# Kernel tuning notes

Measured on AMD Instinct MI355X. Metric: run time of the kernel, lower is better.

Reference implementation:

```python
import jax, jax.numpy as jnp
import numpy as np

N_HEAD, D_MODEL, D_K, D_V, POS_DIM = 8, 512, 64, 64, 2
TEMPERATURE = 8.0
LN_EPS = 1e-6


def setup_inputs() -> dict:
    key = jax.random.key(0)
    ks = jax.random.split(key, 16)
    B, S = 4, 1024
    s = 0.02
    return {
        "q": jax.random.normal(ks[0], (B, S, D_MODEL), jnp.float32),
        "k": jax.random.normal(ks[1], (B, S, D_MODEL), jnp.float32),
        "v": jax.random.normal(ks[2], (B, S, D_MODEL), jnp.float32),
        "pos_mat": jax.random.normal(ks[3], (S, S, POS_DIM), jnp.float32),
        "w_qs": jax.random.normal(ks[4], (N_HEAD * D_K, D_MODEL), jnp.float32) * s,
        "w_ks": jax.random.normal(ks[5], (N_HEAD * D_K, D_MODEL), jnp.float32) * s,
        "w_vs": jax.random.normal(ks[6], (N_HEAD * D_V, D_MODEL), jnp.float32) * s,
        "w_fc": jax.random.normal(ks[7], (D_MODEL, N_HEAD * D_V), jnp.float32) * s,
        "rp_w1": jax.random.normal(ks[8], (D_K, POS_DIM), jnp.float32) * s,
        "rp_b1": jnp.zeros((D_K,), jnp.float32),
        "rp_w2": jax.random.normal(ks[9], (D_K, D_K), jnp.float32) * s,
        "rp_b2": jnp.zeros((D_K,), jnp.float32),
        "ln_g": jnp.ones((D_MODEL,), jnp.float32),
        "ln_b": jnp.zeros((D_MODEL,), jnp.float32),
    }


def reference(q, k, v, pos_mat, w_qs, w_ks, w_vs, w_fc, rp_w1, rp_b1, rp_w2, rp_b2, ln_g, ln_b):
    B, S, _ = q.shape
    residual = q
    # projections -> (b, h, s, d)
    Q = (q @ w_qs.T).reshape(B, S, N_HEAD, D_K).transpose(0, 2, 1, 3)
    K = (k @ w_ks.T).reshape(B, S, N_HEAD, D_K).transpose(0, 2, 1, 3)
    V = (v @ w_vs.T).reshape(B, S, N_HEAD, D_V).transpose(0, 2, 1, 3)
    # relative position embedding: (s, s, d_k)
    a_k = jnp.tanh  # placeholder name avoided; compute MLP (no nonlinearity in original)
    a_k = (pos_mat @ rp_w1.T + rp_b1) @ rp_w2.T + rp_b2
    # sum over d_k of elementwise q*k*a_k, without materializing (b,h,q,k,d)
    attn = jnp.einsum("bhqd,bhkd,qkd->bhqk", Q, K, a_k) / TEMPERATURE
    attn = jax.nn.softmax(attn, axis=-1)  # dropout disabled (eval)
    out = jnp.einsum("bhqk,bhkd->bhqd", attn, V)  # (b,h,s,d_v)
    out = out.transpose(0, 2, 1, 3).reshape(B, S, N_HEAD * D_V)
    out = out @ w_fc.T + residual
    # layer norm
    mu = out.mean(-1, keepdims=True)
    var = out.var(-1, keepdims=True)
    out = (out - mu) / jnp.sqrt(var + LN_EPS) * ln_g + ln_b
    return (out, attn)
```

## Files before the change

### kernel.cpp

```cpp
#include <hip/hip_runtime.h>
#include <math.h>

#define NB   4
#define SEQ  1024
#define DMOD 512
#define NHD  8
#define DK   64

typedef unsigned short ushort_t;
typedef __attribute__((ext_vector_type(8))) short bf16x8;
typedef __attribute__((ext_vector_type(4))) float f32x4;

#define XQ_OFF   1024
#define XK_OFF   (XQ_OFF + 4194304)
#define XV_OFF   (XK_OFF + 4194304)
#define WQ_OFF   (XV_OFF + 4194304)
#define WK_OFF   (WQ_OFF + 524288)
#define WV_OFF   (WK_OFF + 524288)
#define WF_OFF   (WV_OFF + 524288)
#define QBF_OFF  (WF_OFF + 524288)
#define KBF_OFF  (QBF_OFF + 4194304)
#define VT_OFF   (KBF_OFF + 12582912)
#define O2_OFF   XQ_OFF
#define OBF_OFF  XV_OFF
#define POSBF_OFF XQ_OFF

__device__ inline ushort_t f2bf(float x) {
    unsigned u = __builtin_bit_cast(unsigned, x);
    unsigned r = (u + 0x7FFFu + ((u >> 16) & 1u)) >> 16;
    return (ushort_t)r;
}
__device__ inline unsigned pk2(float a, float b) {
    return (unsigned)f2bf(a) | ((unsigned)f2bf(b) << 16);
}

__global__ __launch_bounds__(64)
void prep_kernel(const float* __restrict__ rp_w1, const float* __restrict__ rp_b1,
                 const float* __restrict__ rp_w2, const float* __restrict__ rp_b2,
                 float* __restrict__ ws)
{
    int d = threadIdx.x;
    float w0 = 0.f, w1 = 0.f, cc = 0.f;
    for (int j = 0; j < 64; j++) {
        float r2 = rp_w2[d * 64 + j];
        w0 += r2 * rp_w1[j * 2 + 0];
        w1 += r2 * rp_w1[j * 2 + 1];
        cc += r2 * rp_b1[j];
    }
    ws[d] = cc + rp_b2[d];
    ws[64 + 2 * d + 0] = w0;
    ws[64 + 2 * d + 1] = w1;
}

__global__ __launch_bounds__(256)
void cvt3_kernel(const float* __restrict__ s0, const float* __restrict__ s1,
                 const float* __restrict__ s2, ushort_t* __restrict__ d0,
                 ushort_t* __restrict__ d1, ushort_t* __restrict__ d2)
{
    int t = blockIdx.x * 256 + threadIdx.x;
    const float* s = (blockIdx.y == 0) ? s0 : (blockIdx.y == 1) ? s1 : s2;
    ushort_t* d = (blockIdx.y == 0) ? d0 : (blockIdx.y == 1) ? d1 : d2;
    float4 v = *(const float4*)&s[t * 4];
    uint2 o = {pk2(v.x, v.y), pk2(v.z, v.w)};
    *(uint2*)&d[t * 4] = o;
}

__global__ __launch_bounds__(256)
void cvt4_kernel(const float* __restrict__ s0, const float* __restrict__ s1,
                 const float* __restrict__ s2, const float* __restrict__ s3,
                 ushort_t* __restrict__ d0, ushort_t* __restrict__ d1,
                 ushort_t* __restrict__ d2, ushort_t* __restrict__ d3)
{
    int t = blockIdx.x * 256 + threadIdx.x;
    const float* s = (blockIdx.y == 0) ? s0 : (blockIdx.y == 1) ? s1
                   : (blockIdx.y == 2) ? s2 : s3;
    ushort_t* d = (blockIdx.y == 0) ? d0 : (blockIdx.y == 1) ? d1
                : (blockIdx.y == 2) ? d2 : d3;
    float4 v = *(const float4*)&s[t * 4];
    uint2 o = {pk2(v.x, v.y), pk2(v.z, v.w)};
    *(uint2*)&d[t * 4] = o;
}

__global__ __launch_bounds__(256)
void poscvt_kernel(const float* __restrict__ pos, unsigned* __restrict__ posbf)
{
    int t = blockIdx.x * 256 + threadIdx.x;
    float4 a = *(const float4*)&pos[t * 8];
    float4 b = *(const float4*)&pos[t * 8 + 4];
    uint4 o = {pk2(a.x, a.y), pk2(a.z, a.w), pk2(b.x, b.y), pk2(b.z, b.w)};
    *(uint4*)&posbf[t * 4] = o;
}

#define GP 72
template<int MODE>
__global__ __launch_bounds__(256)
void mfma_gemm(const ushort_t* __restrict__ X, const ushort_t* __restrict__ Wt,
               ushort_t* __restrict__ obf, float* __restrict__ ofp,
               const float* __restrict__ wc, const float* __restrict__ resid)
{
    __shared__ ushort_t Xs[64 * GP];
    __shared__ ushort_t Ws[64 * GP];
    const int n0 = blockIdx.y * 64;
    const int o0 = blockIdx.x * 64;
    const int tid = threadIdx.x;
    const int wave = tid >> 6, lane = tid & 63;
    const int m16 = lane & 15, g = lane >> 4;

    f32x4 acc[4] = {};
    for (int m0 = 0; m0 < 512; m0 += 64) {
        #pragma unroll
        for (int it = 0; it < 2; it++) {
            int idx = tid + it * 256;
            int row = idx >> 3, c8 = (idx & 7) * 8;
            *(uint4*)&Xs[row * GP + c8] = *(const uint4*)&X[(n0 + row) * 512 + m0 + c8];
            *(uint4*)&Ws[row * GP + c8] = *(const uint4*)&Wt[(o0 + row) * 512 + m0 + c8];
        }
        __syncthreads();
        #pragma unroll
        for (int kc = 0; kc < 2; kc++) {
            bf16x8 a = *(const bf16x8*)&Xs[(wave * 16 + m16) * GP + kc * 32 + g * 8];
            #pragma unroll
            for (int to = 0; to < 4; to++) {
                bf16x8 b = *(const bf16x8*)&Ws[(to * 16 + m16) * GP + kc * 32 + g * 8];
                acc[to] = __builtin_amdgcn_mfma_f32_16x16x32_bf16(a, b, acc[to], 0, 0, 0);
            }
        }
        __syncthreads();
    }
    #pragma unroll
    for (int to = 0; to < 4; to++) {
        int o = o0 + to * 16 + m16;
        #pragma unroll
        for (int r = 0; r < 4; r++) {
            int n = n0 + wave * 16 + g * 4 + r;
            float a = acc[to][r];
            int b = n >> 10, s = n & 1023, h = o >> 6, d = o & 63;
            if (MODE == 0) {
                obf[(((b * NHD + h) << 10) + s) * 64 + d] = f2bf(a);
            } else if (MODE == 1) {
                int base = ((((b * NHD + h) << 10) + s) * 192) + d;
                obf[base]       = f2bf(a * wc[d]);
                obf[base + 64]  = f2bf(a * wc[64 + 2 * d + 0]);
                obf[base + 128] = f2bf(a * wc[64 + 2 * d + 1]);
            } else if (MODE == 2) {
                obf[((b * NHD + h) * 64 + d) * 1024 + s] = f2bf(a);
            } else {
                ofp[n * 512 + o] = a + resid[n * 512 + o];
            }
        }
    }
}

#define QPITCH 72
#define KPLANE (64 * QPITCH + 8)
#define POSP 68
__global__ __launch_bounds__(256)
void fused_attn(const ushort_t* __restrict__ Qbf, const ushort_t* __restrict__ Kbf,
                const unsigned* __restrict__ posu, const ushort_t* __restrict__ Vt,
                float* __restrict__ attn, ushort_t* __restrict__ Obf)
{
    __shared__ ushort_t Ks[3 * KPLANE];
    __shared__ ushort_t Vs[64 * QPITCH];
    __shared__ ushort_t Ps[64 * QPITCH];
    __shared__ unsigned PosS[64 * POSP];
    const int bh = blockIdx.x;
    const int q0 = blockIdx.y * 64;
    const int tid = threadIdx.x;
    const int wave = tid >> 6, lane = tid & 63;
    const int m16 = lane & 15, g = lane >> 4;

    const ushort_t* qrow = &Qbf[((bh << 10) + q0 + wave * 16 + m16) * 64];
    bf16x8 qf0 = *(const bf16x8*)&qrow[g * 8];
    bf16x8 qf1 = *(const bf16x8*)&qrow[32 + g * 8];

    float l[4] = {0.f, 0.f, 0.f, 0.f};

    for (int k0 = 0; k0 < 1024; k0 += 64) {
        #pragma unroll
        for (int it = 0; it < 6; it++) {
            int idx = tid + it * 256;
            int row = idx / 24, c = idx % 24;
            int j = c >> 3, d8 = (c & 7) * 8;
            *(uint4*)&Ks[j * KPLANE + row * QPITCH + d8] =
                *(const uint4*)&Kbf[((bh << 10) + k0 + row) * 192 + c * 8];
        }
        #pragma unroll
        for (int it = 0; it < 4; it++) {
            int idx = tid + it * 256;
            int row = idx >> 4, c4 = (idx & 15) * 4;
            *(uint4*)&PosS[row * POSP + c4] =
                *(const uint4*)&posu[(q0 + row) * 1024 + k0 + c4];
        }
        __syncthreads();

        f32x4 sc[4][3] = {};
        #pragma unroll
        for (int kc = 0; kc < 2; kc++) {
            bf16x8 af = kc ? qf1 : qf0;
            #pragma unroll
            for (int tk = 0; tk < 4; tk++)
                #pragma unroll
                for (int j = 0; j < 3; j++) {
                    bf16x8 bfv = *(const bf16x8*)&Ks[j * KPLANE + (tk * 16 + m16) * QPITCH + kc * 32 + g * 8];
                    sc[tk][j] = __builtin_amdgcn_mfma_f32_16x16x32_bf16(af, bfv, sc[tk][j], 0, 0, 0);
                }
        }

        #pragma unroll
        for (int r = 0; r < 4; r++) {
            #pragma unroll
            for (int tk = 0; tk < 4; tk++) {
                unsigned pu = PosS[(wave * 16 + g * 4 + r) * POSP + tk * 16 + m16];
                float p0 = __builtin_bit_cast(float, pu << 16);
                float p1 = __builtin_bit_cast(float, pu & 0xFFFF0000u);
                float s = (sc[tk][0][r] + p0 * sc[tk][1][r] + p1 * sc[tk][2][r]) * 0.125f;
                l[r] += __expf(s);
            }
        }
        __syncthreads();
    }
    float inv_l[4];
    #pragma unroll
    for (int r = 0; r < 4; r++) {
        float s = l[r];
        #pragma unroll
        for (int msk = 1; msk < 16; msk <<= 1) s += __shfl_xor(s, msk, 64);
        inv_l[r] = 1.0f / s;
    }

    f32x4 ao[4] = {};
    for (int k0 = 0; k0 < 1024; k0 += 64) {
        #pragma unroll
        for (int it = 0; it < 6; it++) {
            int idx = tid + it * 256;
            int row = idx / 24, c = idx % 24;
            int j = c >> 3, d8 = (c & 7) * 8;
            *(uint4*)&Ks[j * KPLANE + row * QPITCH + d8] =
                *(const uint4*)&Kbf[((bh << 10) + k0 + row) * 192 + c * 8];
        }
        #pragma unroll
        for (int it = 0; it < 2; it++) {
            int idx = tid + it * 256;
            int row = idx >> 3, c8 = (idx & 7) * 8;
            *(uint4*)&Vs[row * QPITCH + c8] = *(const uint4*)&Vt[(bh * 64 + row) * 1024 + k0 + c8];
        }
        #pragma unroll
        for (int it = 0; it < 4; it++) {
            int idx = tid + it * 256;
            int row = idx >> 4, c4 = (idx & 15) * 4;
            *(uint4*)&PosS[row * POSP + c4] =
                *(const uint4*)&posu[(q0 + row) * 1024 + k0 + c4];
        }
        __syncthreads();

        f32x4 sc[4][3] = {};
        #pragma unroll
        for (int kc = 0; kc < 2; kc++) {
            bf16x8 af = kc ? qf1 : qf0;
            #pragma unroll
            for (int tk = 0; tk < 4; tk++)
                #pragma unroll
                for (int j = 0; j < 3; j++) {
                    bf16x8 bfv = *(const bf16x8*)&Ks[j * KPLANE + (tk * 16 + m16) * QPITCH + kc * 32 + g * 8];
                    sc[tk][j] = __builtin_amdgcn_mfma_f32_16x16x32_bf16(af, bfv, sc[tk][j], 0, 0, 0);
                }
        }

        #pragma unroll
        for (int r = 0; r < 4; r++) {
            int q = q0 + wave * 16 + g * 4 + r;
            #pragma unroll
            for (int tk = 0; tk < 4; tk++) {
                unsigned pu = PosS[(wave * 16 + g * 4 + r) * POSP + tk * 16 + m16];
                float p0 = __builtin_bit_cast(float, pu << 16);
                float p1 = __builtin_bit_cast(float, pu & 0xFFFF0000u);
                float s = (sc[tk][0][r] + p0 * sc[tk][1][r] + p1 * sc[tk][2][r]) * 0.125f;
                float p = __expf(s) * inv_l[r];
                attn[((bh << 10) + q) * 1024 + k0 + tk * 16 + m16] = p;
                Ps[(wave * 16 + g * 4 + r) * QPITCH + tk * 16 + m16] = f2bf(p);
            }
        }
        __syncthreads();

        #pragma unroll
        for (int kc = 0; kc < 2; kc++) {
            bf16x8 a = *(const bf16x8*)&Ps[(wave * 16 + m16) * QPITCH + kc * 32 + g * 8];
            #pragma unroll
            for (int td = 0; td < 4; td++) {
                bf16x8 b = *(const bf16x8*)&Vs[(td * 16 + m16) * QPITCH + kc * 32 + g * 8];
                ao[td] = __builtin_amdgcn_mfma_f32_16x16x32_bf16(a, b, ao[td], 0, 0, 0);
            }
        }
        __syncthreads();
    }

    const int b = bh >> 3, h = bh & 7;
    #pragma unroll
    for (int td = 0; td < 4; td++) {
        int d = td * 16 + m16;
        #pragma unroll
        for (int r = 0; r < 4; r++) {
            int q = q0 + wave * 16 + g * 4 + r;
            Obf[((b << 10) + q) * 512 + h * 64 + d] = f2bf(ao[td][r]);
        }
    }
}

__global__ __launch_bounds__(256)
void ln_kernel(const float* __restrict__ X, const float* __restrict__ g,
               const float* __restrict__ bta, float* __restrict__ out)
{
    const int row = blockIdx.x;
    const int tid = threadIdx.x;
    float2 x = *(const float2*)&X[row * 512 + tid * 2];
    float s  = x.x + x.y;
    float s2 = x.x * x.x + x.y * x.y;
    for (int off = 32; off; off >>= 1) {
        s  += __shfl_down(s, off, 64);
        s2 += __shfl_down(s2, off, 64);
    }
    __shared__ float rs[4], rs2[4];
    __shared__ float mu_s, rstd_s;
    int wave = tid >> 6, lane = tid & 63;
    if (lane == 0) { rs[wave] = s; rs2[wave] = s2; }
    __syncthreads();
    if (tid == 0) {
        float S1 = rs[0] + rs[1] + rs[2] + rs[3];
        float S2 = rs2[0] + rs2[1] + rs2[2] + rs2[3];
        float mu = S1 * (1.0f / 512.0f);
        float var = S2 * (1.0f / 512.0f) - mu * mu;
        mu_s = mu;
        rstd_s = rsqrtf(var + 1e-6f);
    }
    __syncthreads();
    float mu = mu_s, rstd = rstd_s;
    float2 gv = *(const float2*)&g[tid * 2];
    float2 bv = *(const float2*)&bta[tid * 2];
    float2 o;
    o.x = (x.x - mu) * rstd * gv.x + bv.x;
    o.y = (x.y - mu) * rstd * gv.y + bv.y;
    *(float2*)&out[row * 512 + tid * 2] = o;
}

extern "C" void kernel_launch(void* const* d_in, const int* in_sizes, int n_in,
                              void* d_out, int out_size, void* d_ws, size_t ws_size,
                              hipStream_t stream)
{
    const float* q       = (const float*)d_in[0];
    const float* k       = (const float*)d_in[1];
    const float* v       = (const float*)d_in[2];
    const float* pos_mat = (const float*)d_in[3];
    const float* w_qs    = (const float*)d_in[4];
    const float* w_ks    = (const float*)d_in[5];
    const float* w_vs    = (const float*)d_in[6];
    const float* w_fc    = (const float*)d_in[7];
    const float* rp_w1   = (const float*)d_in[8];
    const float* rp_b1   = (const float*)d_in[9];
    const float* rp_w2   = (const float*)d_in[10];
    const float* rp_b2   = (const float*)d_in[11];
    const float* ln_g    = (const float*)d_in[12];
    const float* ln_b    = (const float*)d_in[13];

    char* wsb = (char*)d_ws;
    float*    wc  = (float*)d_ws;
    ushort_t* XQ  = (ushort_t*)(wsb + XQ_OFF);
    ushort_t* XK  = (ushort_t*)(wsb + XK_OFF);
    ushort_t* XV  = (ushort_t*)(wsb + XV_OFF);
    ushort_t* WQ  = (ushort_t*)(wsb + WQ_OFF);
    ushort_t* WK  = (ushort_t*)(wsb + WK_OFF);
    ushort_t* WV  = (ushort_t*)(wsb + WV_OFF);
    ushort_t* WF  = (ushort_t*)(wsb + WF_OFF);
    ushort_t* Qbf = (ushort_t*)(wsb + QBF_OFF);
    ushort_t* Kbf = (ushort_t*)(wsb + KBF_OFF);
    ushort_t* Vt  = (ushort_t*)(wsb + VT_OFF);
    float*    O2  = (float*)(wsb + O2_OFF);
    ushort_t* Obf = (ushort_t*)(wsb + OBF_OFF);
    unsigned* Pbf = (unsigned*)(wsb + POSBF_OFF);

    float* out  = (float*)d_out;
    float* attn = out + 2097152;

    prep_kernel<<<dim3(1), dim3(64), 0, stream>>>(rp_w1, rp_b1, rp_w2, rp_b2, wc);

    cvt3_kernel<<<dim3(2048, 3), 256, 0, stream>>>(q, k, v, XQ, XK, XV);
    cvt4_kernel<<<dim3(256, 4), 256, 0, stream>>>(w_qs, w_ks, w_vs, w_fc, WQ, WK, WV, WF);

    dim3 gp(8, 64);
    mfma_gemm<0><<<gp, 256, 0, stream>>>(XQ, WQ, Qbf, nullptr, nullptr, nullptr);
    poscvt_kernel<<<dim3(1024), 256, 0, stream>>>(pos_mat, Pbf);
    mfma_gemm<1><<<gp, 256, 0, stream>>>(XK, WK, Kbf, nullptr, wc, nullptr);
    mfma_gemm<2><<<gp, 256, 0, stream>>>(XV, WV, Vt, nullptr, nullptr, nullptr);

    fused_attn<<<dim3(32, 16), 256, 0, stream>>>(Qbf, Kbf, Pbf, Vt, attn, Obf);

    mfma_gemm<3><<<gp, 256, 0, stream>>>(Obf, WF, nullptr, O2, nullptr, q);
    ln_kernel<<<dim3(4096), 256, 0, stream>>>(O2, ln_g, ln_b, out);
}
```

Before: 303.1 us.

## Prefetch next K/pos/V tiles into registers while computing the current tile

```diff
diff --git a/kernel.cpp b/kernel.cpp
--- a/kernel.cpp
+++ b/kernel.cpp
@@ -169,29 +169,69 @@
     const int wave = tid >> 6, lane = tid & 63;
     const int m16 = lane & 15, g = lane >> 4;
 
+    const int k_row = (tid % 192) / 24 + (tid / 192) * 8;
+    (void)k_row;
+
     const ushort_t* qrow = &Qbf[((bh << 10) + q0 + wave * 16 + m16) * 64];
     bf16x8 qf0 = *(const bf16x8*)&qrow[g * 8];
     bf16x8 qf1 = *(const bf16x8*)&qrow[32 + g * 8];
 
+    uint4 kreg[6], preg[4], vreg[2];
+
+#define LOAD_K(k0_) \
+    _Pragma("unroll") \
+    for (int it = 0; it < 6; it++) { \
+        int idx = tid + it * 256; \
+        int row = idx / 24, c = idx % 24; \
+        kreg[it] = *(const uint4*)&Kbf[((bh << 10) + (k0_) + row) * 192 + c * 8]; \
+    }
+#define LOAD_P(k0_) \
+    _Pragma("unroll") \
+    for (int it = 0; it < 4; it++) { \
+        int idx = tid + it * 256; \
+        int row = idx >> 4, c4 = (idx & 15) * 4; \
+        preg[it] = *(const uint4*)&posu[(q0 + row) * 1024 + (k0_) + c4]; \
+    }
+#define LOAD_V(k0_) \
+    _Pragma("unroll") \
+    for (int it = 0; it < 2; it++) { \
+        int idx = tid + it * 256; \
+        int row = idx >> 3, c8 = (idx & 7) * 8; \
+        vreg[it] = *(const uint4*)&Vt[(bh * 64 + row) * 1024 + (k0_) + c8]; \
+    }
+#define STORE_K() \
+    _Pragma("unroll") \
+    for (int it = 0; it < 6; it++) { \
+        int idx = tid + it * 256; \
+        int row = idx / 24, c = idx % 24; \
+        int j = c >> 3, d8 = (c & 7) * 8; \
+        *(uint4*)&Ks[j * KPLANE + row * QPITCH + d8] = kreg[it]; \
+    }
+#define STORE_P() \
+    _Pragma("unroll") \
+    for (int it = 0; it < 4; it++) { \
+        int idx = tid + it * 256; \
+        int row = idx >> 4, c4 = (idx & 15) * 4; \
+        *(uint4*)&PosS[row * POSP + c4] = preg[it]; \
+    }
+#define STORE_V() \
+    _Pragma("unroll") \
+    for (int it = 0; it < 2; it++) { \
+        int idx = tid + it * 256; \
+        int row = idx >> 3, c8 = (idx & 7) * 8; \
+        *(uint4*)&Vs[row * QPITCH + c8] = vreg[it]; \
+    }
+
     float l[4] = {0.f, 0.f, 0.f, 0.f};
 
+    LOAD_K(0); LOAD_P(0);
+    STORE_K(); STORE_P();
+    __syncthreads();
     for (int k0 = 0; k0 < 1024; k0 += 64) {
-        #pragma unroll
-        for (int it = 0; it < 6; it++) {
-            int idx = tid + it * 256;
-            int row = idx / 24, c = idx % 24;
-            int j = c >> 3, d8 = (c & 7) * 8;
-            *(uint4*)&Ks[j * KPLANE + row * QPITCH + d8] =
-                *(const uint4*)&Kbf[((bh << 10) + k0 + row) * 192 + c * 8];
-        }
-        #pragma unroll
-        for (int it = 0; it < 4; it++) {
-            int idx = tid + it * 256;
-            int row = idx >> 4, c4 = (idx & 15) * 4;
-            *(uint4*)&PosS[row * POSP + c4] =
-                *(const uint4*)&posu[(q0 + row) * 1024 + k0 + c4];
-        }
-        __syncthreads();
+        const int kn = k0 + 64;
+        if (kn < 1024) {
+            LOAD_K(kn); LOAD_P(kn);
+        }
 
         f32x4 sc[4][3] = {};
         #pragma unroll
@@ -218,6 +258,10 @@
             }
         }
         __syncthreads();
+        if (kn < 1024) {
+            STORE_K(); STORE_P();
+        }
+        __syncthreads();
     }
     float inv_l[4];
     #pragma unroll
@@ -227,31 +271,17 @@
         for (int msk = 1; msk < 16; msk <<= 1) s += __shfl_xor(s, msk, 64);
         inv_l[r] = 1.0f / s;
     }
+    __syncthreads();
 
     f32x4 ao[4] = {};
+    LOAD_K(0); LOAD_P(0); LOAD_V(0);
+    STORE_K(); STORE_P(); STORE_V();
+    __syncthreads();
     for (int k0 = 0; k0 < 1024; k0 += 64) {
-        #pragma unroll
-        for (int it = 0; it < 6; it++) {
-            int idx = tid + it * 256;
-            int row = idx / 24, c = idx % 24;
-            int j = c >> 3, d8 = (c & 7) * 8;
-            *(uint4*)&Ks[j * KPLANE + row * QPITCH + d8] =
-                *(const uint4*)&Kbf[((bh << 10) + k0 + row) * 192 + c * 8];
-        }
-        #pragma unroll
-        for (int it = 0; it < 2; it++) {
-            int idx = tid + it * 256;
-            int row = idx >> 3, c8 = (idx & 7) * 8;
-            *(uint4*)&Vs[row * QPITCH + c8] = *(const uint4*)&Vt[(bh * 64 + row) * 1024 + k0 + c8];
-        }
-        #pragma unroll
-        for (int it = 0; it < 4; it++) {
-            int idx = tid + it * 256;
-            int row = idx >> 4, c4 = (idx & 15) * 4;
-            *(uint4*)&PosS[row * POSP + c4] =
-                *(const uint4*)&posu[(q0 + row) * 1024 + k0 + c4];
-        }
-        __syncthreads();
+        const int kn = k0 + 64;
+        if (kn < 1024) {
+            LOAD_K(kn); LOAD_P(kn); LOAD_V(kn);
+        }
 
         f32x4 sc[4][3] = {};
         #pragma unroll
@@ -292,6 +322,10 @@
             }
         }
         __syncthreads();
+        if (kn < 1024) {
+            STORE_K(); STORE_P(); STORE_V();
+        }
+        __syncthreads();
     }
 
     const int b = bh >> 3, h = bh & 7;
@@ -304,6 +338,12 @@
             Obf[((b << 10) + q) * 512 + h * 64 + d] = f2bf(ao[td][r]);
         }
     }
+#undef LOAD_K
+#undef LOAD_P
+#undef LOAD_V
+#undef STORE_K
+#undef STORE_P
+#undef STORE_V
 }
 
 __global__ __launch_bounds__(256)
```

Result: slower. 413.6 us (+36.4%).

## Fuse fp32-to-bf16 input conversion into a single batched QKV projection GEMM

Applied to the files above, without the earlier changes.

```diff
diff --git a/kernel.cpp b/kernel.cpp
--- a/kernel.cpp
+++ b/kernel.cpp
@@ -21,9 +21,9 @@
 #define QBF_OFF  (WF_OFF + 524288)
 #define KBF_OFF  (QBF_OFF + 4194304)
 #define VT_OFF   (KBF_OFF + 12582912)
+#define POSBF_OFF XQ_OFF
 #define O2_OFF   XQ_OFF
 #define OBF_OFF  XV_OFF
-#define POSBF_OFF XQ_OFF
 
 __device__ inline ushort_t f2bf(float x) {
     unsigned u = __builtin_bit_cast(unsigned, x);
@@ -50,19 +50,6 @@
     ws[d] = cc + rp_b2[d];
     ws[64 + 2 * d + 0] = w0;
     ws[64 + 2 * d + 1] = w1;
-}
-
-__global__ __launch_bounds__(256)
-void cvt3_kernel(const float* __restrict__ s0, const float* __restrict__ s1,
-                 const float* __restrict__ s2, ushort_t* __restrict__ d0,
-                 ushort_t* __restrict__ d1, ushort_t* __restrict__ d2)
-{
-    int t = blockIdx.x * 256 + threadIdx.x;
-    const float* s = (blockIdx.y == 0) ? s0 : (blockIdx.y == 1) ? s1 : s2;
-    ushort_t* d = (blockIdx.y == 0) ? d0 : (blockIdx.y == 1) ? d1 : d2;
-    float4 v = *(const float4*)&s[t * 4];
-    uint2 o = {pk2(v.x, v.y), pk2(v.z, v.w)};
-    *(uint2*)&d[t * 4] = o;
 }
 
 __global__ __launch_bounds__(256)
@@ -92,11 +79,75 @@
 }
 
 #define GP 72
-template<int MODE>
-__global__ __launch_bounds__(256)
-void mfma_gemm(const ushort_t* __restrict__ X, const ushort_t* __restrict__ Wt,
-               ushort_t* __restrict__ obf, float* __restrict__ ofp,
-               const float* __restrict__ wc, const float* __restrict__ resid)
+
+__global__ __launch_bounds__(256)
+void mfma_gemm_qkv(const float* __restrict__ xq, const float* __restrict__ xk,
+                   const float* __restrict__ xv,
+                   const ushort_t* __restrict__ wq, const ushort_t* __restrict__ wk,
+                   const ushort_t* __restrict__ wv,
+                   ushort_t* __restrict__ Qbf, ushort_t* __restrict__ Kbf,
+                   ushort_t* __restrict__ Vt, const float* __restrict__ wc)
+{
+    __shared__ ushort_t Xs[64 * GP];
+    __shared__ ushort_t Ws[64 * GP];
+    const int bz = blockIdx.z;
+    const float* X = (bz == 0) ? xq : (bz == 1) ? xk : xv;
+    const ushort_t* Wt = (bz == 0) ? wq : (bz == 1) ? wk : wv;
+    const int n0 = blockIdx.y * 64;
+    const int o0 = blockIdx.x * 64;
+    const int tid = threadIdx.x;
+    const int wave = tid >> 6, lane = tid & 63;
+    const int m16 = lane & 15, g = lane >> 4;
+
+    f32x4 acc[4] = {};
+    for (int m0 = 0; m0 < 512; m0 += 64) {
+        #pragma unroll
+        for (int it = 0; it < 2; it++) {
+            int idx = tid + it * 256;
+            int row = idx >> 3, c8 = (idx & 7) * 8;
+            float4 a = *(const float4*)&X[(n0 + row) * 512 + m0 + c8];
+            float4 b = *(const float4*)&X[(n0 + row) * 512 + m0 + c8 + 4];
+            uint4 o = {pk2(a.x, a.y), pk2(a.z, a.w), pk2(b.x, b.y), pk2(b.z, b.w)};
+            *(uint4*)&Xs[row * GP + c8] = o;
+            *(uint4*)&Ws[row * GP + c8] = *(const uint4*)&Wt[(o0 + row) * 512 + m0 + c8];
+        }
+        __syncthreads();
+        #pragma unroll
+        for (int kc = 0; kc < 2; kc++) {
+            bf16x8 a = *(const bf16x8*)&Xs[(wave * 16 + m16) * GP + kc * 32 + g * 8];
+            #pragma unroll
+            for (int to = 0; to < 4; to++) {
+                bf16x8 b = *(const bf16x8*)&Ws[(to * 16 + m16) * GP + kc * 32 + g * 8];
+                acc[to] = __builtin_amdgcn_mfma_f32_16x16x32_bf16(a, b, acc[to], 0, 0, 0);
+            }
+        }
+        __syncthreads();
+    }
+    #pragma unroll
+    for (int to = 0; to < 4; to++) {
+        int o = o0 + to * 16 + m16;
+        #pragma unroll
+        for (int r = 0; r < 4; r++) {
+            int n = n0 + wave * 16 + g * 4 + r;
+            float a = acc[to][r];
+            int b = n >> 10, s = n & 1023, h = o >> 6, d = o & 63;
+            if (bz == 0) {
+                Qbf[(((b * NHD + h) << 10) + s) * 64 + d] = f2bf(a);
+            } else if (bz == 1) {
+                int base = ((((b * NHD + h) << 10) + s) * 192) + d;
+                Kbf[base]       = f2bf(a * wc[d]);
+                Kbf[base + 64]  = f2bf(a * wc[64 + 2 * d + 0]);
+                Kbf[base + 128] = f2bf(a * wc[64 + 2 * d + 1]);
+            } else {
+                Vt[((b * NHD + h) * 64 + d) * 1024 + s] = f2bf(a);
+            }
+        }
+    }
+}
+
+__global__ __launch_bounds__(256)
+void mfma_gemm_fc(const ushort_t* __restrict__ X, const ushort_t* __restrict__ Wt,
+                  float* __restrict__ ofp, const float* __restrict__ resid)
 {
     __shared__ ushort_t Xs[64 * GP];
     __shared__ ushort_t Ws[64 * GP];
@@ -133,20 +184,7 @@
         #pragma unroll
         for (int r = 0; r < 4; r++) {
             int n = n0 + wave * 16 + g * 4 + r;
-            float a = acc[to][r];
-            int b = n >> 10, s = n & 1023, h = o >> 6, d = o & 63;
-            if (MODE == 0) {
-                obf[(((b * NHD + h) << 10) + s) * 64 + d] = f2bf(a);
-            } else if (MODE == 1) {
-                int base = ((((b * NHD + h) << 10) + s) * 192) + d;
-                obf[base]       = f2bf(a * wc[d]);
-                obf[base + 64]  = f2bf(a * wc[64 + 2 * d + 0]);
-                obf[base + 128] = f2bf(a * wc[64 + 2 * d + 1]);
-            } else if (MODE == 2) {
-                obf[((b * NHD + h) * 64 + d) * 1024 + s] = f2bf(a);
-            } else {
-                ofp[n * 512 + o] = a + resid[n * 512 + o];
-            }
+            ofp[n * 512 + o] = acc[to][r] + resid[n * 512 + o];
         }
     }
 }
@@ -363,9 +401,6 @@
 
     char* wsb = (char*)d_ws;
     float*    wc  = (float*)d_ws;
-    ushort_t* XQ  = (ushort_t*)(wsb + XQ_OFF);
-    ushort_t* XK  = (ushort_t*)(wsb + XK_OFF);
-    ushort_t* XV  = (ushort_t*)(wsb + XV_OFF);
     ushort_t* WQ  = (ushort_t*)(wsb + WQ_OFF);
     ushort_t* WK  = (ushort_t*)(wsb + WK_OFF);
     ushort_t* WV  = (ushort_t*)(wsb + WV_OFF);
@@ -381,18 +416,14 @@
     float* attn = out + 2097152;
 
     prep_kernel<<<dim3(1), dim3(64), 0, stream>>>(rp_w1, rp_b1, rp_w2, rp_b2, wc);
-
-    cvt3_kernel<<<dim3(2048, 3), 256, 0, stream>>>(q, k, v, XQ, XK, XV);
+    poscvt_kernel<<<dim3(1024), 256, 0, stream>>>(pos_mat, Pbf);
     cvt4_kernel<<<dim3(256, 4), 256, 0, stream>>>(w_qs, w_ks, w_vs, w_fc, WQ, WK, WV, WF);
 
-    dim3 gp(8, 64);
-    mfma_gemm<0><<<gp, 256, 0, stream>>>(XQ, WQ, Qbf, nullptr, nullptr, nullptr);
-    poscvt_kernel<<<dim3(1024), 256, 0, stream>>>(pos_mat, Pbf);
-    mfma_gemm<1><<<gp, 256, 0, stream>>>(XK, WK, Kbf, nullptr, wc, nullptr);
-    mfma_gemm<2><<<gp, 256, 0, stream>>>(XV, WV, Vt, nullptr, nullptr, nullptr);
+    mfma_gemm_qkv<<<dim3(8, 64, 3), 256, 0, stream>>>(q, k, v, WQ, WK, WV,
+                                                      Qbf, Kbf, Vt, wc);
 
     fused_attn<<<dim3(32, 16), 256, 0, stream>>>(Qbf, Kbf, Pbf, Vt, attn, Obf);
 
-    mfma_gemm<3><<<gp, 256, 0, stream>>>(Obf, WF, nullptr, O2, nullptr, q);
+    mfma_gemm_fc<<<dim3(8, 64), 256, 0, stream>>>(Obf, WF, O2, q);
     ln_kernel<<<dim3(4096), 256, 0, stream>>>(O2, ln_g, ln_b, out);
 }
```

After: 296.5 us. 2.2% less time.
